# Performance work log

Measured on AMD Instinct MI355X. Metric: run time of the kernel, lower is better.

## Reference

```python
import jax, jax.numpy as jnp
import numpy as np

NUM_HEADS = 8
SCALE = 25.0
SIM_THRESH = 0.75


def setup_inputs() -> dict:
    key = jax.random.key(0)
    ks = jax.random.split(key, 6)
    B, N, C = 1, 2048, 1024
    x_cls = jax.random.normal(ks[0], (B, N, C), jnp.float32)
    x_reg = jax.random.normal(ks[1], (B, N, C), jnp.float32)
    cls_score = jax.random.uniform(ks[2], (N,), jnp.float32)
    fg_score = jax.random.uniform(ks[3], (N,), jnp.float32)
    W_qkv_cls = jax.random.normal(ks[4], (3 * C, C), jnp.float32) * 0.02
    W_qkv_reg = jax.random.normal(ks[5], (3 * C, C), jnp.float32) * 0.02
    return {"x_cls": x_cls, "x_reg": x_reg, "cls_score": cls_score,
            "fg_score": fg_score, "W_qkv_cls": W_qkv_cls, "W_qkv_reg": W_qkv_reg}


def _l2norm(t):
    return t / jnp.linalg.norm(t, axis=-1, keepdims=True)


def reference(x_cls, x_reg, cls_score, fg_score, W_qkv_cls, W_qkv_reg):
    B, N, C = x_cls.shape
    H = NUM_HEADS
    d = C // H

    def qkv(x, W):
        # (B,N,3C) -> (3,B,H,N,d)
        t = (x @ W.T).reshape(B, N, 3, H, d).transpose(2, 0, 3, 1, 4)
        return t[0], t[1], t[2]

    q_cls, k_cls, v_cls = qkv(x_cls, W_qkv_cls)
    q_reg, k_reg, _ = qkv(x_reg, W_qkv_reg)

    q_cls, k_cls = _l2norm(q_cls), _l2norm(k_cls)
    q_reg, k_reg = _l2norm(q_reg), _l2norm(k_reg)
    v_cls_normed = _l2norm(v_cls)

    # scores broadcast: s[..., i, j] = score[j]; transpose -> score[i]
    s_cls = cls_score.reshape(1, 1, 1, N)
    s_fg = fg_score.reshape(1, 1, 1, N)
    # use_mask=True branch
    m_cls = (s_cls > jnp.swapaxes(s_cls, -2, -1) - 0.1).astype(x_cls.dtype)
    m_fg = (s_fg > jnp.swapaxes(s_fg, -2, -1) - 0.1).astype(x_cls.dtype)

    attn_cls_raw = jnp.einsum('bhid,bhjd->bhij', v_cls_normed, v_cls_normed)

    attn_cls = jax.nn.softmax(
        jnp.einsum('bhid,bhjd->bhij', q_cls, k_cls) * SCALE * s_cls * m_cls, axis=-1)
    attn_reg = jax.nn.softmax(
        jnp.einsum('bhid,bhjd->bhij', q_reg, k_reg) * SCALE * s_fg * m_fg, axis=-1)
    attn = (attn_reg + attn_cls) * 0.5

    x = jnp.einsum('bhij,bhjd->bhid', attn, v_cls).transpose(0, 2, 1, 3).reshape(B, N, C)
    x_ori = v_cls.transpose(0, 2, 1, 3).reshape(B, N, C)
    x_out = jnp.concatenate([x, x_ori], axis=-1)  # (B, N, 2C)

    # ave=True branch (batch 0, head-mean)
    raw = attn_cls_raw.sum(axis=1)[0] / H  # (N, N)
    sim_mask = (raw > SIM_THRESH).astype(x_cls.dtype)
    sim_attn = attn.sum(axis=1)[0] / H
    sim_round2 = jax.nn.softmax(sim_attn, axis=-1)
    sim_round2 = sim_mask * sim_round2
    sim_round2 = sim_round2 / jnp.sum(sim_round2, axis=-1, keepdims=True)
    return x_out, sim_round2
```

## Files before the change

kernel.cpp:

```cpp
#include <hip/hip_runtime.h>


#define NTOK 2048
#define CDIM 1024
#define OD   5120

typedef __attribute__((ext_vector_type(8))) short bf16x8;
typedef __attribute__((ext_vector_type(4))) short s16x4;
typedef __attribute__((ext_vector_type(2))) short s16x2;
typedef __attribute__((ext_vector_type(4))) float f32x4;

#define MFMA16(a,b,c) __builtin_amdgcn_mfma_f32_16x16x32_bf16((a),(b),(c),0,0,0)

__device__ __forceinline__ short f2bf(float x){
  unsigned u = __float_as_uint(x);
  u += 0x7FFFu + ((u >> 16) & 1u);
  return (short)(u >> 16);
}

__device__ __forceinline__ void atomAddF(float* p, float v){
  unsafeAtomicAdd(p, v);
}

__device__ __forceinline__ void gld16(const short* g, short* l){
  __builtin_amdgcn_global_load_lds(
      (const __attribute__((address_space(1))) unsigned int*)g,
      (__attribute__((address_space(3))) unsigned int*)l, 16, 0, 0);
}

__global__ __launch_bounds__(256,8) void k_cvt(
    const float* __restrict__ xc, const float* __restrict__ xr,
    const float* __restrict__ Wc, const float* __restrict__ Wr,
    short* __restrict__ xbc, short* __restrict__ xbr,
    short* __restrict__ wbc, short* __restrict__ wbr)
{
  int idx = blockIdx.x*256 + threadIdx.x;
  const float* src; short* dst; int off;
  if      (idx <  262144){ src = xc; dst = xbc; off = idx; }
  else if (idx <  524288){ src = xr; dst = xbr; off = idx - 262144; }
  else if (idx <  917504){ src = Wc; dst = wbc; off = idx - 524288; }
  else                   { src = Wr; dst = wbr; off = idx - 917504; }
  float4 a = *(const float4*)(src + (size_t)off*8);
  float4 b = *(const float4*)(src + (size_t)off*8 + 4);
  bf16x8 o = { f2bf(a.x), f2bf(a.y), f2bf(a.z), f2bf(a.w),
               f2bf(b.x), f2bf(b.y), f2bf(b.z), f2bf(b.w) };
  *(bf16x8*)(dst + (size_t)off*8) = o;
}

__global__ __launch_bounds__(256,3) void k_qkv(
    const short* __restrict__ xbc, const short* __restrict__ xbr,
    const short* __restrict__ wbc, const short* __restrict__ wbr,
    float* __restrict__ tmp)
{
  const int tid = threadIdx.x;
  const int l   = tid & 63;
  const int w   = tid >> 6;
  const int fr  = l & 15;
  const int fk8 = (l >> 4) * 8;

  const int L     = blockIdx.x;
  const int xcd   = L & 7;
  const int slot  = L >> 3;
  const int panel = xcd*5 + (slot >> 4);
  const int mb    = slot & 15;
  const int m0    = mb * 128;
  const int o0    = panel * 128;

  const short* Xb; const short* Wb; int wrow;
  if (o0 < 3072){ Xb = xbc; Wb = wbc; wrow = o0; }
  else          { Xb = xbr; Wb = wbr; wrow = o0 - 3072; }

  __shared__ __align__(16) short Ab[2][8][64][8];
  __shared__ __align__(16) short Bb[2][8][64][8];

  const int wr = w >> 1;
  const int wc = w & 1;

#define QSTAGE(DB, KN) do {                                                  \
    _Pragma("unroll")                                                        \
    for (int it=0; it<2; ++it){                                              \
      int f = it*4 + w;                                                      \
      gld16(Xb + (size_t)(m0  + f*16 + fr)*CDIM + (KN) + fk8,                \
            &Ab[DB][f][0][0]);                                               \
      gld16(Wb + (size_t)(wrow + f*16 + fr)*CDIM + (KN) + fk8,               \
            &Bb[DB][f][0][0]);                                               \
    }                                                                        \
  } while(0)

  f32x4 acc[4][4] = {};

  QSTAGE(0, 0);
  __syncthreads();

  for (int kt = 0; kt < 32; ++kt){
    const int db = kt & 1;
    if (kt < 31){ if (db) QSTAGE(0, (kt+1)*32); else QSTAGE(1, (kt+1)*32); }
    bf16x8 af[4], bfr[4];
    #pragma unroll
    for (int ai=0;ai<4;ai++) af[ai]  = *(const bf16x8*)&Ab[db][wr*4+ai][l][0];
    #pragma unroll
    for (int bj=0;bj<4;bj++) bfr[bj] = *(const bf16x8*)&Bb[db][wc*4+bj][l][0];
    #pragma unroll
    for (int ai=0;ai<4;ai++)
      #pragma unroll
      for (int bj=0;bj<4;bj++)
        acc[ai][bj] = MFMA16(af[ai], bfr[bj], acc[ai][bj]);
    __syncthreads();
  }
#undef QSTAGE

  #pragma unroll
  for (int ai=0;ai<4;ai++)
    #pragma unroll
    for (int bj=0;bj<4;bj++)
      #pragma unroll
      for (int r=0;r<4;r++)
        tmp[(size_t)(m0 + wr*64 + ai*16 + (l>>4)*4 + r)*OD
            + o0 + wc*64 + bj*16 + fr] = acc[ai][bj][r];
}

__global__ __launch_bounds__(256,4) void k_norm(
    const float* __restrict__ tmp, float* __restrict__ out,
    short* __restrict__ qc, short* __restrict__ kc,
    short* __restrict__ qr, short* __restrict__ kr,
    short* __restrict__ vn, short* __restrict__ vb)
{
  int task = blockIdx.x*4 + (threadIdx.x>>6);
  int lane = threadIdx.x & 63;
  int n = task / 40;
  int rem = task - n*40;
  int chunk = rem >> 3;
  int h = rem & 7;
  const float* src = tmp + (size_t)n*OD + (chunk<<10) + h*128;
  float2 v = *(const float2*)(src + lane*2);
  float ss = v.x*v.x + v.y*v.y;
  #pragma unroll
  for (int m=1;m<64;m<<=1) ss += __shfl_xor(ss, m);
  float rn = 1.0f / sqrtf(ss);
  size_t base = ((size_t)h*NTOK + n)*128 + lane*2;
  s16x2 nv = { f2bf(v.x*rn), f2bf(v.y*rn) };
  switch(chunk){
    case 0: *(s16x2*)&qc[base] = nv; break;
    case 1: *(s16x2*)&kc[base] = nv; break;
    case 3: *(s16x2*)&qr[base] = nv; break;
    case 4: *(s16x2*)&kr[base] = nv; break;
    default: {
      *(s16x2*)&vn[base] = nv;
      *(s16x2*)&vb[base] = (s16x2){ f2bf(v.x), f2bf(v.y) };
      *(float2*)&out[(size_t)n*2048 + 1024 + h*128 + lane*2] = v;
      break;
    }
  }
}

__global__ __launch_bounds__(256,4) void k_vT(
    const short* __restrict__ vb, short* __restrict__ vT)
{
  int b = blockIdx.x;
  int h  = b >> 6;
  int nt = (b >> 1) & 31;
  int dt = b & 1;
  __shared__ short t[64][72];
  int tid = threadIdx.x;
  int r  = tid >> 2;
  int c0 = (tid & 3) << 4;
  #pragma unroll
  for (int u=0;u<2;u++){
    bf16x8 val = *(const bf16x8*)&vb[((size_t)h*NTOK + nt*64 + r)*128 + dt*64 + c0 + u*8];
    #pragma unroll
    for (int e=0;e<8;e++) t[r][c0+u*8+e] = val[e];
  }
  __syncthreads();
  #pragma unroll
  for (int u=0;u<2;u++){
    bf16x8 o;
    #pragma unroll
    for (int e=0;e<8;e++) o[e] = t[c0+u*8+e][r];
    *(bf16x8*)&vT[((size_t)h*128 + dt*64 + r)*NTOK + nt*64 + c0 + u*8] = o;
  }
}

#define JLEN 1024

__global__ __launch_bounds__(256,2) void k_attn(
    const short* __restrict__ qc, const short* __restrict__ kc,
    const short* __restrict__ qr, const short* __restrict__ kr,
    const short* __restrict__ vT,
    const float* __restrict__ csc, const float* __restrict__ fsc,
    float* __restrict__ s_cls, float* __restrict__ s_reg,
    float* __restrict__ Up)
{
  const int tid = threadIdx.x;
  const int l   = tid & 63;
  const int w   = tid >> 6;
  const int L    = blockIdx.x;
  const int xcd  = L & 7;
  const int slot = L >> 3;
  const int hs   = ((slot >> 5) << 3) | xcd;
  const int h    = hs >> 1;
  const int s    = hs & 1;
  const int rem  = slot & 31;
  const int js   = rem >> 4;
  const int ib   = rem & 15;

  const int iw  = ib * 128 + w * 32;
  const int fr  = l & 15;
  const int fk8 = (l >> 4) * 8;
  const size_t hN = (size_t)h * NTOK;
  const size_t hD = (size_t)h * 128;

  const short* Qp = s ? qr : qc;
  const short* Kp = s ? kr : kc;
  const float* sc = s ? fsc : csc;
  float* ssum     = s ? s_reg : s_cls;
  float* Ub       = Up + (size_t)(js*2 + s) * 2097152;

  __shared__ __align__(16) short Kbuf[2][4][4][64][8];
  __shared__ __align__(16) short Vbuf[2][8][2][64][8];
  __shared__ __align__(16) short Ebuf[4][2][2][64][8];

  const int t8 = w * 8;

#define STAGE(DB, JN) do {                                                   \
    _Pragma("unroll")                                                        \
    for (int q8=0; q8<8; ++q8){                                              \
      int t = t8 + q8;                                                       \
      if (t < 16){                                                           \
        int jf = t >> 2, kk = t & 3;                                         \
        gld16(Kp + (hN + (JN) + jf*16 + fr)*128 + kk*32 + fk8,               \
              &Kbuf[DB][jf][kk][0][0]);                                      \
      } else {                                                               \
        int u = t - 16, df = u >> 1, ks = u & 1;                             \
        gld16(vT + (hD + df*16 + fr)*2048 + (JN) + ks*32 + fk8,              \
              &Vbuf[DB][df][ks][0][0]);                                      \
      }                                                                      \
    }                                                                        \
  } while(0)

  bf16x8 aq[2][4];
  #pragma unroll
  for (int i2=0;i2<2;i2++)
    #pragma unroll
    for (int kk=0;kk<4;kk++)
      aq[i2][kk] = *(const bf16x8*)&Qp[(hN + iw + i2*16 + fr)*128 + kk*32 + fk8];

  float sci[2][4];
  #pragma unroll
  for (int i2=0;i2<2;i2++)
    #pragma unroll
    for (int r=0;r<4;r++)
      sci[i2][r] = sc[iw + i2*16 + (l>>4)*4 + r];

  f32x4 U[2][8] = {};
  float p[2][4] = {};

  const int ebyte = l & 7;
  const int ehi   = (l >> 3) & 1;
  const int jbase = js * JLEN;

  STAGE(0, jbase);
  __syncthreads();

  for (int jt = 0; jt < 16; ++jt){
    const int db = jt & 1;
    const int j0 = jbase + jt*64;
    if (jt < 15){ if (db) STAGE(0, j0 + 64); else STAGE(1, j0 + 64); }
    #pragma unroll
    for (int jf=0; jf<4; ++jf){
      f32x4 S0 = {}; f32x4 S1 = {};
      #pragma unroll
      for (int kk=0; kk<4; ++kk){
        bf16x8 b = *(const bf16x8*)&Kbuf[db][jf][kk][l][0];
        S0 = MFMA16(aq[0][kk], b, S0);
        S1 = MFMA16(aq[1][kk], b, S1);
      }
      float sj = sc[j0 + jf*16 + fr];
      float sj25 = 25.0f * sj;
      const int ks  = jf >> 1;
      const int sub = ((jf & 1) << 1) | ehi;
      #pragma unroll
      for (int r=0;r<4;r++){
        float e0 = (sj > sci[0][r]-0.1f) ? __expf(S0[r]*sj25) : 1.0f;
        float e1 = (sj > sci[1][r]-0.1f) ? __expf(S1[r]*sj25) : 1.0f;
        p[0][r] += e0; p[1][r] += e1;
        int lrow = (l>>4)*4 + r + (sub<<4);
        Ebuf[w][0][ks][lrow][ebyte] = f2bf(e0);
        Ebuf[w][1][ks][lrow][ebyte] = f2bf(e1);
      }
    }
    #pragma unroll
    for (int ks=0; ks<2; ++ks){
      bf16x8 ef0 = *(const bf16x8*)&Ebuf[w][0][ks][l][0];
      bf16x8 ef1 = *(const bf16x8*)&Ebuf[w][1][ks][l][0];
      #pragma unroll
      for (int df=0; df<8; ++df){
        bf16x8 bv = *(const bf16x8*)&Vbuf[db][df][ks][l][0];
        U[0][df] = MFMA16(ef0, bv, U[0][df]);
        U[1][df] = MFMA16(ef1, bv, U[1][df]);
      }
    }
    __syncthreads();
  }
#undef STAGE

  #pragma unroll
  for (int m=1;m<16;m<<=1)
    #pragma unroll
    for (int i2=0;i2<2;i2++)
      #pragma unroll
      for (int r=0;r<4;r++) p[i2][r] += __shfl_xor(p[i2][r], m);
  if (fr == 0){
    #pragma unroll
    for (int i2=0;i2<2;i2++)
      #pragma unroll
      for (int r=0;r<4;r++)
        atomAddF(&ssum[hN + iw + i2*16 + (l>>4)*4 + r], p[i2][r]);
  }
  #pragma unroll
  for (int i2=0;i2<2;i2++)
    #pragma unroll
    for (int df=0;df<8;df++)
      #pragma unroll
      for (int r=0;r<4;r++)
        Ub[(hN + iw + i2*16 + (l>>4)*4 + r)*128 + df*16 + fr] = U[i2][df][r];
}

__global__ __launch_bounds__(256,8) void k_attn_fin(
    const float* __restrict__ Up,
    const float* __restrict__ s_cls, const float* __restrict__ s_reg,
    float* __restrict__ out)
{
  int task = blockIdx.x*4 + (threadIdx.x>>6);
  int lane = threadIdx.x & 63;
  int h = task >> 11;
  int row = task & 2047;
  size_t b = (size_t)task*128 + lane*2;
  float2 c0 = *(const float2*)(Up + 0*2097152 + b);
  float2 r0 = *(const float2*)(Up + 1*2097152 + b);
  float2 c1 = *(const float2*)(Up + 2*2097152 + b);
  float2 r1 = *(const float2*)(Up + 3*2097152 + b);
  float isc = 0.5f/s_cls[task];
  float isr = 0.5f/s_reg[task];
  float2 o = { (c0.x+c1.x)*isc + (r0.x+r1.x)*isr,
               (c0.y+c1.y)*isc + (r0.y+r1.y)*isr };
  *(float2*)&out[(size_t)row*2048 + h*128 + lane*2] = o;
}

__global__ __launch_bounds__(256,2) void k_sim(
    const short* __restrict__ qc, const short* __restrict__ kc,
    const short* __restrict__ qr, const short* __restrict__ kr,
    const float* __restrict__ csc, const float* __restrict__ fsc,
    const float* __restrict__ s_cls, const float* __restrict__ s_reg,
    float* __restrict__ out)
{
  const int tid  = threadIdx.x;
  const int lane = tid & 63;
  const int w    = tid >> 6;
  const int i0w  = blockIdx.x * 128 + w * 32;
  const int j0   = blockIdx.y * 64;
  const int fr   = lane & 15;
  const int fk   = (lane >> 4) * 8;

  __shared__ __align__(16) short Bsh[2][16][64][8];

  float sjc[4], sjf[4];
  #pragma unroll
  for (int js=0;js<4;js++){ sjc[js]=csc[j0+js*16+fr]; sjf[js]=fsc[j0+js*16+fr]; }
  int rowb[2]; float sci[2][4], sfi[2][4];
  #pragma unroll
  for (int ri=0;ri<2;ri++){
    rowb[ri] = i0w + ri*16 + ((lane>>4)<<2);
    #pragma unroll
    for (int r=0;r<4;r++){ sci[ri][r]=csc[rowb[ri]+r]; sfi[ri][r]=fsc[rowb[ri]+r]; }
  }

  f32x4 sim[2][4] = {};

  for (int h=0; h<8; ++h){
    const size_t hb = (size_t)h * NTOK;
    bf16x8 aq[2][4], ar[2][4];
    #pragma unroll
    for (int ri=0;ri<2;ri++)
      #pragma unroll
      for (int kk=0;kk<4;kk++){
        aq[ri][kk] = *(const bf16x8*)&qc[(hb + i0w + ri*16 + fr)*128 + kk*32 + fk];
        ar[ri][kk] = *(const bf16x8*)&qr[(hb + i0w + ri*16 + fr)*128 + kk*32 + fk];
      }
    float iscl[2][4], isrl[2][4];
    #pragma unroll
    for (int ri=0;ri<2;ri++)
      #pragma unroll
      for (int r=0;r<4;r++){
        iscl[ri][r] = 1.0f/s_cls[hb + rowb[ri] + r];
        isrl[ri][r] = 1.0f/s_reg[hb + rowb[ri] + r];
      }
    __syncthreads();
    #pragma unroll
    for (int it=0; it<8; ++it){
      int slot = it*256 + tid;
      int str  = slot >> 10;
      int frag = (slot >> 6) & 15;
      int l    = slot & 63;
      int r    = (frag >> 2)*16 + (l & 15);
      int c    = (frag & 3)*32 + (l >> 4)*8;
      const short* gp = (str ? kr : kc) + (hb + j0 + r)*128 + c;
      *(bf16x8*)&Bsh[str][frag][l][0] = *(const bf16x8*)gp;
    }
    __syncthreads();
    #pragma unroll
    for (int js=0; js<4; ++js){
      bf16x8 bc[4], br[4];
      #pragma unroll
      for (int kk=0;kk<4;kk++){
        bc[kk] = *(const bf16x8*)&Bsh[0][js*4+kk][lane][0];
        br[kk] = *(const bf16x8*)&Bsh[1][js*4+kk][lane][0];
      }
      #pragma unroll
      for (int ri=0;ri<2;ri++){
        f32x4 Sc = {}; f32x4 Sr = {};
        #pragma unroll
        for (int kk=0;kk<4;kk++){
          Sc = MFMA16(aq[ri][kk], bc[kk], Sc);
          Sr = MFMA16(ar[ri][kk], br[kk], Sr);
        }
        #pragma unroll
        for (int r=0;r<4;r++){
          float ec = (sjc[js] > sci[ri][r]-0.1f) ? __expf(Sc[r]*(25.0f*sjc[js])) : 1.0f;
          float er = (sjf[js] > sfi[ri][r]-0.1f) ? __expf(Sr[r]*(25.0f*sjf[js])) : 1.0f;
          sim[ri][js][r] += ec*iscl[ri][r] + er*isrl[ri][r];
        }
      }
    }
  }
  #pragma unroll
  for (int ri=0;ri<2;ri++)
    #pragma unroll
    for (int js=0;js<4;js++)
      #pragma unroll
      for (int r=0;r<4;r++)
        out[4194304ull + (size_t)(rowb[ri]+r)*2048 + j0 + js*16 + fr]
            = sim[ri][js][r] * 0.0625f;
}

__global__ __launch_bounds__(256,4) void k_raw(
    const short* __restrict__ vn, unsigned char* __restrict__ mask)
{
  const int tid  = threadIdx.x;
  const int lane = tid & 63;
  const int w    = tid >> 6;
  const int i0w  = blockIdx.x * 128 + w * 32;
  const int j0   = blockIdx.y * 64;
  const int fr   = lane & 15;
  const int fk   = (lane >> 4) * 8;

  __shared__ __align__(16) short Bsh[16][64][8];

  f32x4 raw[2][4] = {};

  for (int cc=0; cc<8; ++cc){
    const size_t hb = (size_t)cc * NTOK;
    bf16x8 av[2][4];
    #pragma unroll
    for (int ri=0;ri<2;ri++)
      #pragma unroll
      for (int kk=0;kk<4;kk++)
        av[ri][kk] = *(const bf16x8*)&vn[(hb + i0w + ri*16 + fr)*128 + kk*32 + fk];
    __syncthreads();
    #pragma unroll
    for (int it=0; it<4; ++it){
      int slot = it*256 + tid;
      int frag = (slot >> 6) & 15;
      int l    = slot & 63;
      int r    = (frag >> 2)*16 + (l & 15);
      int c    = (frag & 3)*32 + (l >> 4)*8;
      *(bf16x8*)&Bsh[frag][l][0] = *(const bf16x8*)&vn[(hb + j0 + r)*128 + c];
    }
    __syncthreads();
    #pragma unroll
    for (int js=0; js<4; ++js){
      bf16x8 bv[4];
      #pragma unroll
      for (int kk=0;kk<4;kk++) bv[kk] = *(const bf16x8*)&Bsh[js*4+kk][lane][0];
      #pragma unroll
      for (int ri=0;ri<2;ri++)
        #pragma unroll
        for (int kk=0;kk<4;kk++)
          raw[ri][js] = MFMA16(av[ri][kk], bv[kk], raw[ri][js]);
    }
  }
  const int rb0 = i0w + ((lane>>4)<<2);
  #pragma unroll
  for (int ri=0;ri<2;ri++)
    #pragma unroll
    for (int js=0;js<4;js++)
      #pragma unroll
      for (int r=0;r<4;r++)
        mask[(size_t)(rb0 + ri*16 + r)*2048 + j0 + js*16 + fr]
            = raw[ri][js][r] > 6.0f ? 1 : 0;
}

__global__ __launch_bounds__(256,4) void k_final(
    float* __restrict__ out, const unsigned char* __restrict__ mask)
{
  int row  = blockIdx.x*4 + (threadIdx.x>>6);
  int lane = threadIdx.x & 63;
  float* sr = out + 4194304ull + (size_t)row*2048;
  const unsigned char* mr = mask + (size_t)row*2048;
  float v[32];
  float sum2 = 0.0f;
  #pragma unroll
  for (int c=0;c<32;c++){
    float e = __expf(sr[c*64 + lane]);
    v[c] = (mr[c*64 + lane] != 0) ? e : 0.0f;
    sum2 += v[c];
  }
  #pragma unroll
  for (int m=1;m<64;m<<=1) sum2 += __shfl_xor(sum2, m);
  float inv = 1.0f / sum2;
  #pragma unroll
  for (int c=0;c<32;c++) sr[c*64 + lane] = v[c]*inv;
}

extern "C" void kernel_launch(void* const* d_in, const int* in_sizes, int n_in,
                              void* d_out, int out_size, void* d_ws, size_t ws_size,
                              hipStream_t stream)
{
  const float* xcls = (const float*)d_in[0];
  const float* xreg = (const float*)d_in[1];
  const float* csc  = (const float*)d_in[2];
  const float* fsc  = (const float*)d_in[3];
  const float* Wc   = (const float*)d_in[4];
  const float* Wr   = (const float*)d_in[5];
  float* out = (float*)d_out;

  char* ws = (char*)d_ws;
  float* tmp          = (float*)ws;
  unsigned char* mask = (unsigned char*)ws;
  char* accbase       = ws + 4u*1024*1024;
  float* s_cls        = (float*)(accbase);
  float* s_reg        = (float*)(accbase + 65536);
  float* Up           = (float*)(accbase + 131072);
  short* qc = (short*)(ws + 41943040ull);
  short* kc = qc + 2097152;
  short* qr = kc + 2097152;
  short* kr = qr + 2097152;
  short* vn = kr + 2097152;
  short* vb = vn + 2097152;
  short* vT = vb + 2097152;
  short* xbc = (short*)(ws + 41943040ull);
  short* xbr = xbc + 2097152;
  short* wbc = xbr + 2097152;
  short* wbr = wbc + 3145728;

  k_cvt  <<<4608,        256, 0, stream>>>(xcls, xreg, Wc, Wr, xbc, xbr, wbc, wbr);
  k_qkv  <<<640,         256, 0, stream>>>(xbc, xbr, wbc, wbr, tmp);
  k_norm <<<20480,       256, 0, stream>>>(tmp, out, qc, kc, qr, kr, vn, vb);
  k_vT   <<<512,         256, 0, stream>>>(vb, vT);
  hipMemsetAsync(accbase, 0, 131072, stream);
  k_attn <<<512,         256, 0, stream>>>(qc, kc, qr, kr, vT, csc, fsc,
                                           s_cls, s_reg, Up);
  k_attn_fin <<<4096,    256, 0, stream>>>(Up, s_cls, s_reg, out);
  k_raw  <<<dim3(16,32), 256, 0, stream>>>(vn, mask);
  k_sim  <<<dim3(16,32), 256, 0, stream>>>(qc, kc, qr, kr, csc, fsc, s_cls, s_reg, out);
  k_final<<<512,         256, 0, stream>>>(out, mask);
}
```

Before: 254.8 us.

## Compute transposed QK^T and pass exp tiles via bpermute instead of LDS

The QK^T MFMA now has swapped operands, so each lane holds scores for one query row across four key columns. The exponentials are packed to bf16 with v_cvt_pk_bf16_f32 and rearranged into the PV A-operand layout with ds_bpermute, which removes the Ebuf shared-memory write/read round trip and the per-element f2bf. Row sums now need fewer shuffles, and s_setprio raises priority around the MFMA blocks. In exchange it adds cross-lane permutes and selects in the inner loop.

```diff
diff --git a/kernel.cpp b/kernel.cpp
--- a/kernel.cpp
+++ b/kernel.cpp
@@ -16,6 +16,12 @@
   unsigned u = __float_as_uint(x);
   u += 0x7FFFu + ((u >> 16) & 1u);
   return (short)(u >> 16);
+}
+
+__device__ __forceinline__ int cvtpk(float lo, float hi){
+  int r;
+  asm("v_cvt_pk_bf16_f32 %0, %1, %2" : "=v"(r) : "v"(lo), "v"(hi));
+  return r;
 }
 
 __device__ __forceinline__ void atomAddF(float* p, float v){
@@ -205,7 +211,8 @@
 
   const int iw  = ib * 128 + w * 32;
   const int fr  = l & 15;
-  const int fk8 = (l >> 4) * 8;
+  const int g   = l >> 4;
+  const int fk8 = g * 8;
   const size_t hN = (size_t)h * NTOK;
   const size_t hD = (size_t)h * 128;
 
@@ -217,7 +224,6 @@
 
   __shared__ __align__(16) short Kbuf[2][4][4][64][8];
   __shared__ __align__(16) short Vbuf[2][8][2][64][8];
-  __shared__ __align__(16) short Ebuf[4][2][2][64][8];
 
   const int t8 = w * 8;
 
@@ -237,25 +243,23 @@
     }                                                                        \
   } while(0)
 
-  bf16x8 aq[2][4];
+  bf16x8 bq[2][4];
   #pragma unroll
   for (int i2=0;i2<2;i2++)
     #pragma unroll
     for (int kk=0;kk<4;kk++)
-      aq[i2][kk] = *(const bf16x8*)&Qp[(hN + iw + i2*16 + fr)*128 + kk*32 + fk8];
-
-  float sci[2][4];
-  #pragma unroll
-  for (int i2=0;i2<2;i2++)
-    #pragma unroll
-    for (int r=0;r<4;r++)
-      sci[i2][r] = sc[iw + i2*16 + (l>>4)*4 + r];
+      bq[i2][kk] = *(const bf16x8*)&Qp[(hN + iw + i2*16 + fr)*128 + kk*32 + fk8];
+
+  float sci[2];
+  sci[0] = sc[iw + fr] - 0.1f;
+  sci[1] = sc[iw + 16 + fr] - 0.1f;
 
   f32x4 U[2][8] = {};
-  float p[2][4] = {};
-
-  const int ebyte = l & 7;
-  const int ehi   = (l >> 3) & 1;
+  float p[2] = {0.f, 0.f};
+
+  const int srcA = ((((g<<1)    & 3) << 4) + fr) << 2;
+  const int srcB = ((((g<<1 | 1)& 3) << 4) + fr) << 2;
+  const bool ghi = g >= 2;
   const int jbase = js * JLEN;
 
   STAGE(0, jbase);
@@ -266,63 +270,80 @@
     const int j0 = jbase + jt*64;
     if (jt < 15){ if (db) STAGE(0, j0 + 64); else STAGE(1, j0 + 64); }
     #pragma unroll
-    for (int jf=0; jf<4; ++jf){
-      f32x4 S0 = {}; f32x4 S1 = {};
-      #pragma unroll
-      for (int kk=0; kk<4; ++kk){
-        bf16x8 b = *(const bf16x8*)&Kbuf[db][jf][kk][l][0];
-        S0 = MFMA16(aq[0][kk], b, S0);
-        S1 = MFMA16(aq[1][kk], b, S1);
-      }
-      float sj = sc[j0 + jf*16 + fr];
-      float sj25 = 25.0f * sj;
-      const int ks  = jf >> 1;
-      const int sub = ((jf & 1) << 1) | ehi;
-      #pragma unroll
-      for (int r=0;r<4;r++){
-        float e0 = (sj > sci[0][r]-0.1f) ? __expf(S0[r]*sj25) : 1.0f;
-        float e1 = (sj > sci[1][r]-0.1f) ? __expf(S1[r]*sj25) : 1.0f;
-        p[0][r] += e0; p[1][r] += e1;
-        int lrow = (l>>4)*4 + r + (sub<<4);
-        Ebuf[w][0][ks][lrow][ebyte] = f2bf(e0);
-        Ebuf[w][1][ks][lrow][ebyte] = f2bf(e1);
-      }
-    }
-    #pragma unroll
     for (int ks=0; ks<2; ++ks){
-      bf16x8 ef0 = *(const bf16x8*)&Ebuf[w][0][ks][l][0];
-      bf16x8 ef1 = *(const bf16x8*)&Ebuf[w][1][ks][l][0];
+      int cpk[2][2][2];
+      #pragma unroll
+      for (int t=0; t<2; ++t){
+        const int jf = ks*2 + t;
+        f32x4 S0 = {}; f32x4 S1 = {};
+        __builtin_amdgcn_s_setprio(1);
+        #pragma unroll
+        for (int kk=0; kk<4; ++kk){
+          bf16x8 kb = *(const bf16x8*)&Kbuf[db][jf][kk][l][0];
+          S0 = MFMA16(kb, bq[0][kk], S0);
+          S1 = MFMA16(kb, bq[1][kk], S1);
+        }
+        __builtin_amdgcn_s_setprio(0);
+        float4 sjv = *(const float4*)&sc[j0 + jf*16 + 4*g];
+        float e0[4], e1[4];
+        #pragma unroll
+        for (int r=0;r<4;r++){
+          float sj = (&sjv.x)[r];
+          float sj25 = 25.0f * sj;
+          e0[r] = (sj > sci[0]) ? __expf(S0[r]*sj25) : 1.0f;
+          e1[r] = (sj > sci[1]) ? __expf(S1[r]*sj25) : 1.0f;
+          p[0] += e0[r]; p[1] += e1[r];
+        }
+        cpk[0][t][0] = cvtpk(e0[0], e0[1]);
+        cpk[0][t][1] = cvtpk(e0[2], e0[3]);
+        cpk[1][t][0] = cvtpk(e1[0], e1[1]);
+        cpk[1][t][1] = cvtpk(e1[2], e1[3]);
+      }
+      bf16x8 ea[2];
+      #pragma unroll
+      for (int i2=0;i2<2;i2++){
+        int a0 = __builtin_amdgcn_ds_bpermute(srcA, cpk[i2][0][0]);
+        int a1 = __builtin_amdgcn_ds_bpermute(srcA, cpk[i2][0][1]);
+        int a2 = __builtin_amdgcn_ds_bpermute(srcA, cpk[i2][1][0]);
+        int a3 = __builtin_amdgcn_ds_bpermute(srcA, cpk[i2][1][1]);
+        int b0 = __builtin_amdgcn_ds_bpermute(srcB, cpk[i2][0][0]);
+        int b1 = __builtin_amdgcn_ds_bpermute(srcB, cpk[i2][0][1]);
+        int b2 = __builtin_amdgcn_ds_bpermute(srcB, cpk[i2][1][0]);
+        int b3 = __builtin_amdgcn_ds_bpermute(srcB, cpk[i2][1][1]);
+        int wd[4];
+        wd[0] = ghi ? a2 : a0;  wd[1] = ghi ? a3 : a1;
+        wd[2] = ghi ? b2 : b0;  wd[3] = ghi ? b3 : b1;
+        ea[i2] = *(bf16x8*)wd;
+      }
+      __builtin_amdgcn_s_setprio(1);
       #pragma unroll
       for (int df=0; df<8; ++df){
         bf16x8 bv = *(const bf16x8*)&Vbuf[db][df][ks][l][0];
-        U[0][df] = MFMA16(ef0, bv, U[0][df]);
-        U[1][df] = MFMA16(ef1, bv, U[1][df]);
-      }
+        U[0][df] = MFMA16(ea[0], bv, U[0][df]);
+        U[1][df] = MFMA16(ea[1], bv, U[1][df]);
+      }
+      __builtin_amdgcn_s_setprio(0);
     }
     __syncthreads();
   }
 #undef STAGE
 
   #pragma unroll
-  for (int m=1;m<16;m<<=1)
-    #pragma unroll
-    for (int i2=0;i2<2;i2++)
-      #pragma unroll
-      for (int r=0;r<4;r++) p[i2][r] += __shfl_xor(p[i2][r], m);
-  if (fr == 0){
-    #pragma unroll
-    for (int i2=0;i2<2;i2++)
+  for (int i2=0;i2<2;i2++){
+    p[i2] += __shfl_xor(p[i2], 16);
+    p[i2] += __shfl_xor(p[i2], 32);
+  }
+  if (l < 16){
+    atomAddF(&ssum[hN + iw + l],      p[0]);
+    atomAddF(&ssum[hN + iw + 16 + l], p[1]);
+  }
+  #pragma unroll
+  for (int i2=0;i2<2;i2++)
+    #pragma unroll
+    for (int df=0;df<8;df++)
       #pragma unroll
       for (int r=0;r<4;r++)
-        atomAddF(&ssum[hN + iw + i2*16 + (l>>4)*4 + r], p[i2][r]);
-  }
-  #pragma unroll
-  for (int i2=0;i2<2;i2++)
-    #pragma unroll
-    for (int df=0;df<8;df++)
-      #pragma unroll
-      for (int r=0;r<4;r++)
-        Ub[(hN + iw + i2*16 + (l>>4)*4 + r)*128 + df*16 + fr] = U[i2][df][r];
+        Ub[(hN + iw + i2*16 + g*4 + r)*128 + df*16 + fr] = U[i2][df][r];
 }
 
 __global__ __launch_bounds__(256,8) void k_attn_fin(
```

Result: no change. 259.2 us (+1.7%).
